# Kernel tuning notes

Hardware: AMD Instinct MI355X
Metric: run time of the kernel (lower is better)

Reference implementation:

```python
import jax, jax.numpy as jnp
import numpy as np


def setup_inputs() -> dict:
    key = jax.random.key(0)
    ks = jax.random.split(key, 16)
    N, F_in, C, E = 50000, 128, 64, 800000
    H = 2 * C      # hidden width of first GCN layer = 128
    P = 128        # num_proj_hidden
    K = 3          # cluster_num (hardcoded in GRACE)

    def lin(kw, fan_in, fan_out):
        # torch Linear default init: U(-1/sqrt(fan_in), 1/sqrt(fan_in))
        bound = 1.0 / np.sqrt(fan_in)
        return jax.random.uniform(kw, (fan_in, fan_out), jnp.float32, -bound, bound)

    inp = {
        "x1": jax.random.normal(ks[0], (N, F_in), jnp.float32),
        "edge_index1": jax.random.randint(ks[1], (2, E), 0, N, jnp.int64 if jax.config.jax_enable_x64 else jnp.int32),
        "x2": jax.random.normal(ks[2], (N, F_in), jnp.float32),
        "edge_index2": jax.random.randint(ks[3], (2, E), 0, N, jnp.int64 if jax.config.jax_enable_x64 else jnp.int32),
        # encoder GCN layers
        "W1": lin(ks[4], F_in, H), "b1": jnp.zeros((H,), jnp.float32),
        "W2": lin(ks[5], H, C),    "b2": jnp.zeros((C,), jnp.float32),
        # instance projector: Linear(C,C) -> ReLU -> Linear(C,P)
        "Wp1": lin(ks[6], C, C), "bp1": jnp.zeros((C,), jnp.float32),
        "Wp2": lin(ks[7], C, P), "bp2": jnp.zeros((P,), jnp.float32),
        # cluster projector: Linear(C,C) -> ReLU -> Linear(C,K) -> Softmax
        "Wc1": lin(ks[8], C, C), "bc1": jnp.zeros((C,), jnp.float32),
        "Wc2": lin(ks[9], C, K), "bc2": jnp.zeros((K,), jnp.float32),
    }
    return inp


def _gcn_encoder(x, edge_index, W1, b1, W2, b2):
    N = x.shape[0]
    loop = jnp.arange(N, dtype=edge_index.dtype)
    row = jnp.concatenate([edge_index[0], loop])  # message sources (x_j)
    col = jnp.concatenate([edge_index[1], loop])  # aggregation targets
    deg = jax.ops.segment_sum(jnp.ones_like(col, jnp.float32), col, num_segments=N)
    dinv = jax.lax.rsqrt(deg)  # deg >= 1 due to self loops
    norm = dinv[row] * dinv[col]  # [E+N]

    def layer(h, W, b):
        h = h @ W  # transform first (PyG GCNConv), [N, F_out]
        msg = h[row] * norm[:, None]  # gather + scale, [E+N, F_out]
        return jax.ops.segment_sum(msg, col, num_segments=N) + b

    h = jax.nn.relu(layer(x, W1, b1))
    h = jax.nn.relu(layer(h, W2, b2))
    return h


def _l2norm(z, eps=1e-12):
    # matches F.normalize(z, dim=1): x / max(||x||, eps)
    n = jnp.sqrt(jnp.sum(z * z, axis=1, keepdims=True))
    return z / jnp.maximum(n, eps)


def reference(x1, edge_index1, x2, edge_index2,
              W1, b1, W2, b2, Wp1, bp1, Wp2, bp2, Wc1, bc1, Wc2, bc2):
    z1 = _gcn_encoder(x1, edge_index1, W1, b1, W2, b2)
    z2 = _gcn_encoder(x2, edge_index2, W1, b1, W2, b2)

    inst = lambda z: _l2norm(jax.nn.relu(z @ Wp1 + bp1) @ Wp2 + bp2)
    clus = lambda z: jax.nn.softmax(jax.nn.relu(z @ Wc1 + bc1) @ Wc2 + bc2, axis=1)

    z_i = inst(z1)
    z_j = inst(z2)
    c_i = clus(z1)
    c_j = clus(z2)
    return (z_i, z_j, c_i, c_j)
```

## Files before the change

kernel.cpp:

```cpp
#include <hip/hip_runtime.h>
#include <cstdint>
#include <cstddef>

using u16 = unsigned short;
using u32 = unsigned int;

typedef __bf16 bf16x8 __attribute__((ext_vector_type(8)));
typedef float  f32x4  __attribute__((ext_vector_type(4)));

__device__ __forceinline__ float bf2f(u16 b) { union { u32 i; float f; } v; v.i = ((u32)b) << 16; return v.f; }
__device__ __forceinline__ u16 f2bf(float f) { __bf16 b = (__bf16)f; return __builtin_bit_cast(u16, b); }
__device__ __forceinline__ float bflo(u32 u) { union { u32 i; float f; } v; v.i = u << 16; return v.f; }
__device__ __forceinline__ float bfhi(u32 u) { union { u32 i; float f; } v; v.i = u & 0xffff0000u; return v.f; }
__device__ __forceinline__ u32 pack2(float a, float b) { return (u32)f2bf(a) | ((u32)f2bf(b) << 16); }

__device__ __forceinline__ void dot2acc(float& acc, u32 hv, u32 sel) {
    asm("v_dot2_f32_bf16 %0, %1, %2, %0" : "+v"(acc) : "v"(hv), "v"(sel));
}

__device__ __forceinline__ float loadx(const void* p, size_t i, int flag_bf16) {
    return flag_bf16 ? bf2f(((const u16*)p)[i]) : ((const float*)p)[i];
}
__device__ __forceinline__ void storex(void* p, size_t i, float v, int flag_bf16) {
    if (flag_bf16) ((u16*)p)[i] = f2bf(v);
    else           ((float*)p)[i] = v;
}

__device__ __forceinline__ bf16x8 load_afrag_ext(const void* A, size_t off, int flag) {
    if (flag) return *reinterpret_cast<const bf16x8*>((const u16*)A + off);
    const float* f = (const float*)A + off;
    float4 a = *reinterpret_cast<const float4*>(f);
    float4 b = *reinterpret_cast<const float4*>(f + 4);
    bf16x8 r;
    r[0] = (__bf16)a.x; r[1] = (__bf16)a.y; r[2] = (__bf16)a.z; r[3] = (__bf16)a.w;
    r[4] = (__bf16)b.x; r[5] = (__bf16)b.y; r[6] = (__bf16)b.z; r[7] = (__bf16)b.w;
    return r;
}

__global__ void k_detect(const u32* __restrict__ x, int* __restrict__ flag) {
    int lane = threadIdx.x;
    u32 u = x[lane];
    int e = (u >> 7) & 0xFF;
    int hit = (e >= 100 && e <= 145) ? 1 : 0;
    unsigned long long b = __ballot(hit);
    if (lane == 0) flag[0] = (__popcll(b) >= 32) ? 1 : 0;
}

struct ConvJob { const void* src; float* dst; int n; };
struct ConvJobs { ConvJob j[12]; };

__global__ void k_wconv(ConvJobs jobs, const int* __restrict__ flagp) {
    const int f = *flagp;
    const int stride = gridDim.x * blockDim.x;
    for (int s = 0; s < 12; ++s) {
        const ConvJob jb = jobs.j[s];
        for (int i = blockIdx.x * blockDim.x + threadIdx.x; i < jb.n; i += stride)
            jb.dst[i] = loadx(jb.src, i, f);
    }
}

struct TJob { const float* W; u16* WT; int K, NC; };
struct TJobs { TJob j[5]; };

__global__ void k_wtrans(TJobs jobs) {
    const int stride = gridDim.x * blockDim.x;
    for (int s = 0; s < 5; ++s) {
        const TJob jb = jobs.j[s];
        const int tot = jb.K * jb.NC;
        for (int i = blockIdx.x * blockDim.x + threadIdx.x; i < tot; i += stride) {
            int k = i / jb.NC, n = i - k * jb.NC;
            jb.WT[n * jb.K + k] = f2bf(jb.W[i]);
        }
    }
}

static const int CAPSH = 12;
static const int OVCAP = 65536;

__global__ __launch_bounds__(256) void k_bin(const int* __restrict__ ei0, const int* __restrict__ ei1,
                                             int* __restrict__ cur, u32* __restrict__ stage,
                                             int2* __restrict__ ov, int* __restrict__ ocnt,
                                             int E, int NB, int nblk) {
    const int g = blockIdx.y;
    const int* ei = g ? ei1 : ei0;
    const int chunk = (E + nblk - 1) / nblk;
    const int e0 = blockIdx.x * chunk;
    const int e1 = (e0 + chunk < E) ? e0 + chunk : E;
    const int tid = threadIdx.x;
    __shared__ int h[512];
    __shared__ int lb[512];
    for (int i = tid; i < NB; i += 256) h[i] = 0;
    __syncthreads();
    for (int e = e0 + tid; e < e1; e += 256) {
        int d = __builtin_nontemporal_load(ei + E + e);
        atomicAdd(&h[d >> 7], 1);
    }
    __syncthreads();
    for (int b = tid; b < NB; b += 256) {
        int c = h[b];
        lb[b] = c ? atomicAdd(&cur[g * NB + b], c) : 0;
    }
    __syncthreads();
    for (int i = tid; i < NB; i += 256) h[i] = 0;
    __syncthreads();
    for (int e = e0 + tid; e < e1; e += 256) {
        int s = __builtin_nontemporal_load(ei + e);
        int d = ei[E + e];
        int b = d >> 7;
        int p = lb[b] + atomicAdd(&h[b], 1);
        if (p < (1 << CAPSH)) {
            stage[((size_t)(g * NB + b) << CAPSH) + p] = (u32)s | ((u32)(d & 127) << 16);
        } else {
            int oi = atomicAdd(ocnt, 1);
            if (oi < OVCAP) ov[oi] = make_int2(s, d | (g << 24));
        }
    }
}

__global__ __launch_bounds__(256) void k_bscan(const int* __restrict__ cur, const int2* __restrict__ ov,
                                               const int* __restrict__ ocnt, int* __restrict__ bbase,
                                               int* __restrict__ rowptr, int N, int E, int NB) {
    __shared__ int tot[2][512];
    const int tid = threadIdx.x;
    for (int g = 0; g < 2; ++g)
        for (int i = tid; i < 512; i += 256) {
            int s = 0;
            if (i < NB) {
                int cv = cur[g * NB + i];
                s = (cv < (1 << CAPSH)) ? cv : (1 << CAPSH);
            }
            tot[g][i] = s;
        }
    __syncthreads();
    int no = *ocnt; if (no > OVCAP) no = OVCAP;
    for (int i = tid; i < no; i += 256) {
        int y = ov[i].y;
        atomicAdd(&tot[y >> 24][(y & 0xFFFFFF) >> 7], 1);
    }
    __syncthreads();
    int o00 = tot[0][tid], o01 = tot[0][tid + 256];
    int o10 = tot[1][tid], o11 = tot[1][tid + 256];
    for (int off = 1; off < 512; off <<= 1) {
        int a0 = tot[0][tid]       + ((tid >= off)       ? tot[0][tid - off]       : 0);
        int a1 = tot[0][tid + 256] + ((tid + 256 >= off) ? tot[0][tid + 256 - off] : 0);
        int b0 = tot[1][tid]       + ((tid >= off)       ? tot[1][tid - off]       : 0);
        int b1 = tot[1][tid + 256] + ((tid + 256 >= off) ? tot[1][tid + 256 - off] : 0);
        __syncthreads();
        tot[0][tid] = a0; tot[0][tid + 256] = a1;
        tot[1][tid] = b0; tot[1][tid + 256] = b1;
        __syncthreads();
    }
    if (tid < NB)       { bbase[tid]            = tot[0][tid] - o00;       bbase[NB + tid]       = tot[1][tid] - o10; }
    if (tid + 256 < NB) { bbase[tid + 256]      = tot[0][tid + 256] - o01; bbase[NB + tid + 256] = tot[1][tid + 256] - o11; }
    if (tid == 0) {
        rowptr[N] = E;
        rowptr[(size_t)(N + 1) + N] = E;
    }
}

__global__ __launch_bounds__(256) void k_scatter(const int* __restrict__ cur, const u32* __restrict__ stage,
                                                 const int2* __restrict__ ov, const int* __restrict__ ocnt,
                                                 const int* __restrict__ bbase, int* __restrict__ rowptr,
                                                 float* __restrict__ dinv, int* __restrict__ csr,
                                                 int N, int E, int NB) {
    const int g = blockIdx.y, b = blockIdx.x, tid = threadIdx.x;
    const int lo = b << 7;
    int R = N - lo; if (R > 128) R = 128;
    __shared__ int hist[128], scn[128], curs[128];
    if (tid < 128) hist[tid] = 0;
    __syncthreads();
    int cv = cur[g * NB + b];
    const int n = (cv < (1 << CAPSH)) ? cv : (1 << CAPSH);
    const u32* sp = stage + ((size_t)(g * NB + b) << CAPSH);
    for (int i = tid; i < n; i += 256) atomicAdd(&hist[sp[i] >> 16], 1);
    int no = *ocnt; if (no > OVCAP) no = OVCAP;
    for (int i = tid; i < no; i += 256) {
        int y = ov[i].y;
        if ((y >> 24) != g) continue;
        int d = y & 0xFFFFFF;
        if (d >= lo && d < lo + 128) atomicAdd(&hist[d - lo], 1);
    }
    __syncthreads();
    int orig = (tid < 128) ? hist[tid] : 0;
    if (tid < 128) scn[tid] = orig;
    __syncthreads();
    for (int off = 1; off < 128; off <<= 1) {
        int v = 0;
        if (tid < 128) v = scn[tid] + ((tid >= off) ? scn[tid - off] : 0);
        __syncthreads();
        if (tid < 128) scn[tid] = v;
        __syncthreads();
    }
    const int base = bbase[g * NB + b];
    if (tid < R) {
        int ex = base + scn[tid] - orig;
        rowptr[(size_t)g * (N + 1) + lo + tid] = ex;
        curs[tid] = ex;
        dinv[(size_t)g * N + lo + tid] = rsqrtf((float)(orig + 1));
    }
    __syncthreads();
    int* out = csr + (size_t)g * E;
    for (int i = tid; i < n; i += 256) {
        u32 v = sp[i];
        int pos = atomicAdd(&curs[v >> 16], 1);
        out[pos] = (int)(v & 0xFFFFu);
    }
    for (int i = tid; i < no; i += 256) {
        int y = ov[i].y;
        if ((y >> 24) != g) continue;
        int d = y & 0xFFFFFF;
        if (d >= lo && d < lo + 128) {
            int pos = atomicAdd(&curs[d - lo], 1);
            out[pos] = ov[i].x;
        }
    }
}

template <int K, int NC, bool AEXT, bool BIAS, bool RELU, bool NORM, bool OEXT, bool SCALE, int ARS>
__global__ __launch_bounds__(256) void k_mgemm(const void* __restrict__ A0, const void* __restrict__ A1,
                                               size_t astride, const u16* __restrict__ WT,
                                               const float* __restrict__ bias, void* __restrict__ outv,
                                               size_t out_off, size_t ostride, int M,
                                               const int* __restrict__ flagp,
                                               const float* __restrict__ dvp) {
    constexpr int NT = NC / 16;
    constexpr int KI = K / 32;
    constexpr int RS = (ARS == 0) ? K : ARS;
    const int flag = *flagp;
    const int g = blockIdx.y;
    const void* Av = g ? A1 : A0;
    const int lane = threadIdx.x & 63;
    const int wave = threadIdx.x >> 6;
    const int q = lane >> 4;
    const int c = lane & 15;
    const int m0 = blockIdx.x * 64 + wave * 16;
    int arow = m0 + c;
    if (arow > M - 1) arow = M - 1;
    const size_t abase = (size_t)g * astride + (size_t)arow * RS;

    bf16x8 afr[KI];
#pragma unroll
    for (int ki = 0; ki < KI; ++ki) {
        size_t off = abase + (size_t)ki * 32 + q * 8;
        if (AEXT) afr[ki] = load_afrag_ext(Av, off, flag);
        else      afr[ki] = *reinterpret_cast<const bf16x8*>((const u16*)Av + off);
    }

    f32x4 acc[NT];
#pragma unroll
    for (int t = 0; t < NT; ++t) acc[t] = (f32x4){0.f, 0.f, 0.f, 0.f};

#pragma unroll
    for (int ki = 0; ki < KI; ++ki) {
#pragma unroll
        for (int t = 0; t < NT; ++t) {
            const u16* bptr = WT + (size_t)(t * 16 + c) * K + ki * 32 + q * 8;
            bf16x8 bfr = *reinterpret_cast<const bf16x8*>(bptr);
            acc[t] = __builtin_amdgcn_mfma_f32_16x16x32_bf16(afr[ki], bfr, acc[t], 0, 0, 0);
        }
    }

#pragma unroll
    for (int t = 0; t < NT; ++t) {
        float bv = BIAS ? bias[t * 16 + c] : 0.f;
#pragma unroll
        for (int r = 0; r < 4; ++r) {
            float v = acc[t][r] + bv;
            if (RELU) v = fmaxf(v, 0.f);
            acc[t][r] = v;
        }
    }

    if constexpr (NORM) {
        float ss[4] = {0.f, 0.f, 0.f, 0.f};
#pragma unroll
        for (int t = 0; t < NT; ++t)
#pragma unroll
            for (int r = 0; r < 4; ++r) ss[r] += acc[t][r] * acc[t][r];
#pragma unroll
        for (int r = 0; r < 4; ++r) {
#pragma unroll
            for (int m = 1; m < 16; m <<= 1) ss[r] += __shfl_xor(ss[r], m, 64);
            float s = 1.f / fmaxf(sqrtf(ss[r]), 1e-12f);
#pragma unroll
            for (int t = 0; t < NT; ++t) acc[t][r] *= s;
        }
    }

    const size_t obase = out_off + (size_t)g * ostride;
#pragma unroll
    for (int r = 0; r < 4; ++r) {
        const int grow = m0 + q * 4 + r;
        if (grow < M) {
            float sc = 1.f;
            if constexpr (SCALE) sc = dvp[(size_t)g * M + grow];
#pragma unroll
            for (int t = 0; t < NT; ++t) {
                float v = SCALE ? acc[t][r] * sc : acc[t][r];
                size_t oi = obase + (size_t)grow * NC + t * 16 + c;
                if (OEXT) storex(outv, oi, v, flag);
                else      ((u16*)outv)[oi] = f2bf(v);
            }
        }
    }
}

__global__ __launch_bounds__(256) void k_agg128(const u32* __restrict__ H, const int* __restrict__ rowptr,
                                                const int* __restrict__ csr, const float* __restrict__ dinv,
                                                const float* __restrict__ bias, u32* __restrict__ out,
                                                int N, int E, int Q) {
    const u32 SL = 0x00003f80u, SH = 0x3f800000u;
    const int bid = blockIdx.x;
    const int role = bid & 7;
    const int g = role >> 2;
    const int sub = role & 3;
    const int nl = (bid >> 3) * 4 + (threadIdx.x >> 6);
    if (nl >= Q) return;
    const int node = sub * Q + nl;
    if (node >= N) return;
    const int lane = threadIdx.x & 63;
    const int half = lane >> 5;
    const int w = lane & 31;
    const u32* h2 = H + (size_t)g * N * 64 + 2 * w;
    const int* rp = rowptr + (size_t)g * (N + 1);
    const int* cs = csr + (size_t)g * E;
    const float dn = dinv[(size_t)g * N + node];
    int e = rp[node];
    const int end = rp[node + 1];
    float a0 = 0.f, a1 = 0.f, a2 = 0.f, a3 = 0.f;
    if (half == 0) {
        uint2 sv = *reinterpret_cast<const uint2*>(h2 + (size_t)node * 64);
        dot2acc(a0, sv.x, SL); dot2acc(a1, sv.x, SH);
        dot2acc(a2, sv.y, SL); dot2acc(a3, sv.y, SH);
    }
    while (e < end) {
        int cnt = end - e; if (cnt > 64) cnt = 64;
        int my = (lane < cnt) ? cs[e + lane] : 0;
        int j = 0;
        for (; j + 8 <= cnt; j += 8) {
            int s0 = __shfl(my, j + half, 64);
            int s1 = __shfl(my, j + 2 + half, 64);
            int s2 = __shfl(my, j + 4 + half, 64);
            int s3 = __shfl(my, j + 6 + half, 64);
            uint2 h0 = *reinterpret_cast<const uint2*>(h2 + (size_t)s0 * 64);
            uint2 h1 = *reinterpret_cast<const uint2*>(h2 + (size_t)s1 * 64);
            uint2 hh2 = *reinterpret_cast<const uint2*>(h2 + (size_t)s2 * 64);
            uint2 h3 = *reinterpret_cast<const uint2*>(h2 + (size_t)s3 * 64);
            dot2acc(a0, h0.x, SL); dot2acc(a1, h0.x, SH); dot2acc(a2, h0.y, SL); dot2acc(a3, h0.y, SH);
            dot2acc(a0, h1.x, SL); dot2acc(a1, h1.x, SH); dot2acc(a2, h1.y, SL); dot2acc(a3, h1.y, SH);
            dot2acc(a0, hh2.x, SL); dot2acc(a1, hh2.x, SH); dot2acc(a2, hh2.y, SL); dot2acc(a3, hh2.y, SH);
            dot2acc(a0, h3.x, SL); dot2acc(a1, h3.x, SH); dot2acc(a2, h3.y, SL); dot2acc(a3, h3.y, SH);
        }
        for (; j < cnt; j += 2) {
            int idx = j + half;
            int src = __shfl(my, idx < cnt ? idx : 0, 64);
            if (idx < cnt) {
                uint2 hv = *reinterpret_cast<const uint2*>(h2 + (size_t)src * 64);
                dot2acc(a0, hv.x, SL); dot2acc(a1, hv.x, SH);
                dot2acc(a2, hv.y, SL); dot2acc(a3, hv.y, SH);
            }
        }
        e += cnt;
    }
    a0 += __shfl_xor(a0, 32, 64);
    a1 += __shfl_xor(a1, 32, 64);
    a2 += __shfl_xor(a2, 32, 64);
    a3 += __shfl_xor(a3, 32, 64);
    float x = half ? a2 : a0;
    float y = half ? a3 : a1;
    const int c0 = 4 * w + 2 * half;
    float r0 = fmaxf(x * dn + bias[c0], 0.f);
    float r1 = fmaxf(y * dn + bias[c0 + 1], 0.f);
    out[((size_t)g * N + node) * 64 + 2 * w + half] = pack2(r0, r1);
}

__global__ __launch_bounds__(256) void k_agg64(const u32* __restrict__ H, const int* __restrict__ rowptr,
                                               const int* __restrict__ csr, const float* __restrict__ dinv,
                                               const float* __restrict__ bias, u32* __restrict__ out,
                                               int N, int E, int Q) {
    const u32 SL = 0x00003f80u, SH = 0x3f800000u;
    const int bid = blockIdx.x;
    const int role = bid & 7;
    const int g = role >> 2;
    const int sub = role & 3;
    const int nl = (bid >> 3) * 4 + (threadIdx.x >> 6);
    if (nl >= Q) return;
    const int node = sub * Q + nl;
    if (node >= N) return;
    const int lane = threadIdx.x & 63;
    const int quad = lane >> 4;
    const int w = lane & 15;
    const u32* h2 = H + (size_t)g * N * 32 + 2 * w;
    const int* rp = rowptr + (size_t)g * (N + 1);
    const int* cs = csr + (size_t)g * E;
    const float dn = dinv[(size_t)g * N + node];
    int e = rp[node];
    const int end = rp[node + 1];
    float a0 = 0.f, a1 = 0.f, a2 = 0.f, a3 = 0.f;
    if (quad == 0) {
        uint2 sv = *reinterpret_cast<const uint2*>(h2 + (size_t)node * 32);
        dot2acc(a0, sv.x, SL); dot2acc(a1, sv.x, SH);
        dot2acc(a2, sv.y, SL); dot2acc(a3, sv.y, SH);
    }
    while (e < end) {
        int cnt = end - e; if (cnt > 64) cnt = 64;
        int my = (lane < cnt) ? cs[e + lane] : 0;
        int j = 0;
        for (; j + 16 <= cnt; j += 16) {
            int s0 = __shfl(my, j + quad, 64);
            int s1 = __shfl(my, j + 4 + quad, 64);
            int s2 = __shfl(my, j + 8 + quad, 64);
            int s3 = __shfl(my, j + 12 + quad, 64);
            uint2 h0 = *reinterpret_cast<const uint2*>(h2 + (size_t)s0 * 32);
            uint2 h1 = *reinterpret_cast<const uint2*>(h2 + (size_t)s1 * 32);
            uint2 hh2 = *reinterpret_cast<const uint2*>(h2 + (size_t)s2 * 32);
            uint2 h3 = *reinterpret_cast<const uint2*>(h2 + (size_t)s3 * 32);
            dot2acc(a0, h0.x, SL); dot2acc(a1, h0.x, SH); dot2acc(a2, h0.y, SL); dot2acc(a3, h0.y, SH);
            dot2acc(a0, h1.x, SL); dot2acc(a1, h1.x, SH); dot2acc(a2, h1.y, SL); dot2acc(a3, h1.y, SH);
            dot2acc(a0, hh2.x, SL); dot2acc(a1, hh2.x, SH); dot2acc(a2, hh2.y, SL); dot2acc(a3, hh2.y, SH);
            dot2acc(a0, h3.x, SL); dot2acc(a1, h3.x, SH); dot2acc(a2, h3.y, SL); dot2acc(a3, h3.y, SH);
        }
        for (; j < cnt; j += 4) {
            int idx = j + quad;
            int src = __shfl(my, idx < cnt ? idx : 0, 64);
            if (idx < cnt) {
                uint2 hv = *reinterpret_cast<const uint2*>(h2 + (size_t)src * 32);
                dot2acc(a0, hv.x, SL); dot2acc(a1, hv.x, SH);
                dot2acc(a2, hv.y, SL); dot2acc(a3, hv.y, SH);
            }
        }
        e += cnt;
    }
    a0 += __shfl_xor(a0, 16, 64); a0 += __shfl_xor(a0, 32, 64);
    a1 += __shfl_xor(a1, 16, 64); a1 += __shfl_xor(a1, 32, 64);
    a2 += __shfl_xor(a2, 16, 64); a2 += __shfl_xor(a2, 32, 64);
    a3 += __shfl_xor(a3, 16, 64); a3 += __shfl_xor(a3, 32, 64);
    if (quad < 2) {
        float x = quad ? a2 : a0;
        float y = quad ? a3 : a1;
        const int c0 = 4 * w + 2 * quad;
        float r0 = fmaxf(x * dn + bias[c0], 0.f);
        float r1 = fmaxf(y * dn + bias[c0 + 1], 0.f);
        out[((size_t)g * N + node) * 32 + 2 * w + quad] = pack2(r0, r1);
    }
}

__global__ __launch_bounds__(256) void k_clus(const u16* __restrict__ v, const float* __restrict__ Wc2,
                                              const float* __restrict__ bc2, void* __restrict__ outv,
                                              size_t out_off, size_t ostride, int N,
                                              const int* __restrict__ flagp) {
    const int g = blockIdx.y;
    const int node = blockIdx.x * 4 + (threadIdx.x >> 6);
    if (node >= N) return;
    const int flag = *flagp;
    const int lane = threadIdx.x & 63;
    float ul = bf2f(v[((size_t)g * N + node) * 128 + 64 + lane]);
    float a0 = ul * Wc2[lane * 3 + 0];
    float a1 = ul * Wc2[lane * 3 + 1];
    float a2 = ul * Wc2[lane * 3 + 2];
#pragma unroll
    for (int m = 1; m < 64; m <<= 1) {
        a0 += __shfl_xor(a0, m, 64);
        a1 += __shfl_xor(a1, m, 64);
        a2 += __shfl_xor(a2, m, 64);
    }
    a0 += bc2[0]; a1 += bc2[1]; a2 += bc2[2];
    float mx = fmaxf(a0, fmaxf(a1, a2));
    float e0 = expf(a0 - mx), e1 = expf(a1 - mx), e2 = expf(a2 - mx);
    float inv = 1.f / (e0 + e1 + e2);
    if (lane < 3) {
        float r = (lane == 0) ? e0 : ((lane == 1) ? e1 : e2);
        storex(outv, out_off + (size_t)g * ostride + (size_t)node * 3 + lane, r * inv, flag);
    }
}

extern "C" void kernel_launch(void* const* d_in, const int* in_sizes, int n_in,
                              void* d_out, int out_size, void* d_ws, size_t ws_size,
                              hipStream_t stream) {
    const int N = in_sizes[0] / 128;
    const int E = in_sizes[1] / 2;
    const int* ei0 = (const int*)d_in[1];
    const int* ei1 = (const int*)d_in[3];
    const int NB = (N + 127) >> 7;

    size_t off = 0;
    auto alloc = [&](size_t bytes) -> void* {
        void* p = (char*)d_ws + off;
        off += (bytes + 255) & ~(size_t)255;
        return p;
    };
    int* flag = (int*)alloc(256);
    const int wcnt[12] = {128 * 128, 128, 128 * 64, 64, 64 * 64, 64, 64 * 128, 128, 64 * 64, 64, 64 * 3, 3};
    float* wf[12];
    for (int i = 0; i < 12; ++i) {
        if (i == 5) { wf[5] = (float*)alloc(128 * 4); continue; }
        if (i == 9) { wf[9] = wf[5] + 64; continue; }
        wf[i] = (float*)alloc((size_t)wcnt[i] * 4);
    }
    float* b1f = wf[1]; float* b2f = wf[3]; float* bpcf = wf[5]; float* bp2f = wf[7];
    float* Wc2f = wf[10]; float* bc2f = wf[11];
    u16* W1T  = (u16*)alloc(128 * 128 * 2);
    u16* W2T  = (u16*)alloc(64 * 128 * 2);
    u16* Wp1T = (u16*)alloc(64 * 64 * 2);
    u16* Wc1T = (u16*)alloc(64 * 64 * 2);
    u16* Wp2T = (u16*)alloc(128 * 64 * 2);
    u16* WpcT = Wp1T;

    const int ncell = 2 * NB;
    int* cur    = (int*)alloc((size_t)(ncell + 1) * 4);
    int* ocnt   = cur + ncell;
    int2* ov    = (int2*)alloc((size_t)OVCAP * 8);
    u32* stage  = (u32*)alloc(((size_t)ncell << CAPSH) * 4);
    int* bbase  = (int*)alloc((size_t)2 * NB * 4);
    int* rowptr = (int*)alloc((size_t)2 * (N + 1) * 4);
    float* dinv = (float*)alloc((size_t)2 * N * 4);
    int* csr    = (int*)alloc((size_t)2 * E * 4);
    u16* A1 = (u16*)alloc((size_t)2 * N * 128 * 2);
    u16* H2 = A1;
    u16* Qb = (u16*)alloc((size_t)2 * N * 128 * 2);
    u16* U2 = Qb;
    u16* Z  = (u16*)alloc((size_t)2 * N * 64 * 2);
    (void)ws_size; (void)n_in; (void)out_size;

    k_detect<<<1, 64, 0, stream>>>((const u32*)d_in[0], flag);
    ConvJobs jobs;
    for (int i = 0; i < 12; ++i) jobs.j[i] = ConvJob{d_in[4 + i], wf[i], wcnt[i]};
    k_wconv<<<64, 256, 0, stream>>>(jobs, flag);
    TJobs tj;
    tj.j[0] = TJob{wf[0], W1T, 128, 128};
    tj.j[1] = TJob{wf[2], W2T, 128, 64};
    tj.j[2] = TJob{wf[4], Wp1T, 64, 64};
    tj.j[3] = TJob{wf[8], Wc1T, 64, 64};
    tj.j[4] = TJob{wf[6], Wp2T, 64, 128};
    k_wtrans<<<40, 256, 0, stream>>>(tj);

    hipMemsetAsync(cur, 0, (size_t)(ncell + 1) * 4, stream);
    const int NBLK = 128;
    k_bin<<<dim3(NBLK, 2), 256, 0, stream>>>(ei0, ei1, cur, stage, ov, ocnt, E, NB, NBLK);
    k_bscan<<<1, 256, 0, stream>>>(cur, ov, ocnt, bbase, rowptr, N, E, NB);
    k_scatter<<<dim3(NB, 2), 256, 0, stream>>>(cur, stage, ov, ocnt, bbase, rowptr, dinv, csr, N, E, NB);

    const dim3 gM((N + 63) / 64, 2);
    const dim3 gA((N + 3) / 4, 2);
    const int Q = (N + 3) / 4;
    const dim3 gAgg(8 * ((Q + 3) / 4));

    k_mgemm<128, 128, true, false, false, false, false, true, 0><<<gM, 256, 0, stream>>>(
        d_in[0], d_in[2], 0, W1T, nullptr, A1, 0, (size_t)N * 128, N, flag, dinv);
    k_agg128<<<gAgg, 256, 0, stream>>>((const u32*)A1, rowptr, csr, dinv, b1f, (u32*)Qb, N, E, Q);
    k_mgemm<128, 64, false, false, false, false, false, true, 0><<<gM, 256, 0, stream>>>(
        Qb, Qb, (size_t)N * 128, W2T, nullptr, H2, 0, (size_t)N * 64, N, flag, dinv);
    k_agg64<<<gAgg, 256, 0, stream>>>((const u32*)H2, rowptr, csr, dinv, b2f, (u32*)Z, N, E, Q);

    k_mgemm<64, 128, false, true, true, false, false, false, 0><<<gM, 256, 0, stream>>>(
        Z, Z, (size_t)N * 64, WpcT, bpcf, U2, 0, (size_t)N * 128, N, flag, nullptr);
    k_mgemm<64, 128, false, true, false, true, true, false, 128><<<gM, 256, 0, stream>>>(
        U2, U2, (size_t)N * 128, Wp2T, bp2f, d_out, 0, (size_t)N * 128, N, flag, nullptr);
    k_clus<<<gA, 256, 0, stream>>>(U2, Wc2f, bc2f, d_out,
                                   (size_t)2 * N * 128, (size_t)N * 3, N, flag);
}
```

Baseline: 404.8 us.

## Fuse first-layer aggregation with second-layer GEMM via LDS tile and MFMA

The layer-1 aggregation kernel now handles 16 nodes per block (4 per wave). It writes the ReLU'd bf16 rows into a swizzled LDS tile, then multiplies that tile by W2T with MFMA 16x16x32 and scales by dinv to produce H2 directly. This removes a separate GEMM launch and the write and re-read of the 128-wide intermediate, and H2 moves to the Qb buffer. In exchange each wave processes four nodes sequentially, which may lower parallelism and latency hiding in the gather, and a block barrier is added.

```diff
diff --git a/kernel.cpp b/kernel.cpp
--- a/kernel.cpp
+++ b/kernel.cpp
@@ -305,73 +305,107 @@
     }
 }
 
-__global__ __launch_bounds__(256) void k_agg128(const u32* __restrict__ H, const int* __restrict__ rowptr,
-                                                const int* __restrict__ csr, const float* __restrict__ dinv,
-                                                const float* __restrict__ bias, u32* __restrict__ out,
-                                                int N, int E, int Q) {
+__global__ __launch_bounds__(256) void k_agg128f(const u32* __restrict__ H, const int* __restrict__ rowptr,
+                                                 const int* __restrict__ csr, const float* __restrict__ dinv,
+                                                 const float* __restrict__ bias, const u16* __restrict__ W2T,
+                                                 u16* __restrict__ H2, int N, int E, int Q) {
     const u32 SL = 0x00003f80u, SH = 0x3f800000u;
     const int bid = blockIdx.x;
     const int role = bid & 7;
     const int g = role >> 2;
     const int sub = role & 3;
-    const int nl = (bid >> 3) * 4 + (threadIdx.x >> 6);
-    if (nl >= Q) return;
-    const int node = sub * Q + nl;
-    if (node >= N) return;
+    const int blk16 = bid >> 3;
     const int lane = threadIdx.x & 63;
+    const int wv = threadIdx.x >> 6;
     const int half = lane >> 5;
     const int w = lane & 31;
     const u32* h2 = H + (size_t)g * N * 64 + 2 * w;
     const int* rp = rowptr + (size_t)g * (N + 1);
     const int* cs = csr + (size_t)g * E;
-    const float dn = dinv[(size_t)g * N + node];
-    int e = rp[node];
-    const int end = rp[node + 1];
-    float a0 = 0.f, a1 = 0.f, a2 = 0.f, a3 = 0.f;
-    if (half == 0) {
-        uint2 sv = *reinterpret_cast<const uint2*>(h2 + (size_t)node * 64);
-        dot2acc(a0, sv.x, SL); dot2acc(a1, sv.x, SH);
-        dot2acc(a2, sv.y, SL); dot2acc(a3, sv.y, SH);
-    }
-    while (e < end) {
-        int cnt = end - e; if (cnt > 64) cnt = 64;
-        int my = (lane < cnt) ? cs[e + lane] : 0;
-        int j = 0;
-        for (; j + 8 <= cnt; j += 8) {
-            int s0 = __shfl(my, j + half, 64);
-            int s1 = __shfl(my, j + 2 + half, 64);
-            int s2 = __shfl(my, j + 4 + half, 64);
-            int s3 = __shfl(my, j + 6 + half, 64);
-            uint2 h0 = *reinterpret_cast<const uint2*>(h2 + (size_t)s0 * 64);
-            uint2 h1 = *reinterpret_cast<const uint2*>(h2 + (size_t)s1 * 64);
-            uint2 hh2 = *reinterpret_cast<const uint2*>(h2 + (size_t)s2 * 64);
-            uint2 h3 = *reinterpret_cast<const uint2*>(h2 + (size_t)s3 * 64);
-            dot2acc(a0, h0.x, SL); dot2acc(a1, h0.x, SH); dot2acc(a2, h0.y, SL); dot2acc(a3, h0.y, SH);
-            dot2acc(a0, h1.x, SL); dot2acc(a1, h1.x, SH); dot2acc(a2, h1.y, SL); dot2acc(a3, h1.y, SH);
-            dot2acc(a0, hh2.x, SL); dot2acc(a1, hh2.x, SH); dot2acc(a2, hh2.y, SL); dot2acc(a3, hh2.y, SH);
-            dot2acc(a0, h3.x, SL); dot2acc(a1, h3.x, SH); dot2acc(a2, h3.y, SL); dot2acc(a3, h3.y, SH);
-        }
-        for (; j < cnt; j += 2) {
-            int idx = j + half;
-            int src = __shfl(my, idx < cnt ? idx : 0, 64);
-            if (idx < cnt) {
-                uint2 hv = *reinterpret_cast<const uint2*>(h2 + (size_t)src * 64);
-                dot2acc(a0, hv.x, SL); dot2acc(a1, hv.x, SH);
-                dot2acc(a2, hv.y, SL); dot2acc(a3, hv.y, SH);
+
+    __shared__ __align__(16) u32 qlds[16][64];
+
+#pragma unroll
+    for (int i = 0; i < 4; ++i) {
+        const int tr = wv * 4 + i;
+        const int nl = blk16 * 16 + tr;
+        const bool valid = (nl < Q) && (sub * Q + nl < N);
+        const int node = valid ? sub * Q + nl : 0;
+        const float dn = dinv[(size_t)g * N + node];
+        int e = rp[node];
+        const int end = rp[node + 1];
+        float a0 = 0.f, a1 = 0.f, a2 = 0.f, a3 = 0.f;
+        if (half == 0) {
+            uint2 sv = *reinterpret_cast<const uint2*>(h2 + (size_t)node * 64);
+            dot2acc(a0, sv.x, SL); dot2acc(a1, sv.x, SH);
+            dot2acc(a2, sv.y, SL); dot2acc(a3, sv.y, SH);
+        }
+        while (e < end) {
+            int cnt = end - e; if (cnt > 64) cnt = 64;
+            int my = (lane < cnt) ? cs[e + lane] : 0;
+            int j = 0;
+            for (; j + 8 <= cnt; j += 8) {
+                int s0 = __shfl(my, j + half, 64);
+                int s1 = __shfl(my, j + 2 + half, 64);
+                int s2 = __shfl(my, j + 4 + half, 64);
+                int s3 = __shfl(my, j + 6 + half, 64);
+                uint2 h0 = *reinterpret_cast<const uint2*>(h2 + (size_t)s0 * 64);
+                uint2 h1 = *reinterpret_cast<const uint2*>(h2 + (size_t)s1 * 64);
+                uint2 hh2 = *reinterpret_cast<const uint2*>(h2 + (size_t)s2 * 64);
+                uint2 h3 = *reinterpret_cast<const uint2*>(h2 + (size_t)s3 * 64);
+                dot2acc(a0, h0.x, SL); dot2acc(a1, h0.x, SH); dot2acc(a2, h0.y, SL); dot2acc(a3, h0.y, SH);
+                dot2acc(a0, h1.x, SL); dot2acc(a1, h1.x, SH); dot2acc(a2, h1.y, SL); dot2acc(a3, h1.y, SH);
+                dot2acc(a0, hh2.x, SL); dot2acc(a1, hh2.x, SH); dot2acc(a2, hh2.y, SL); dot2acc(a3, hh2.y, SH);
+                dot2acc(a0, h3.x, SL); dot2acc(a1, h3.x, SH); dot2acc(a2, h3.y, SL); dot2acc(a3, h3.y, SH);
             }
-        }
-        e += cnt;
-    }
-    a0 += __shfl_xor(a0, 32, 64);
-    a1 += __shfl_xor(a1, 32, 64);
-    a2 += __shfl_xor(a2, 32, 64);
-    a3 += __shfl_xor(a3, 32, 64);
-    float x = half ? a2 : a0;
-    float y = half ? a3 : a1;
-    const int c0 = 4 * w + 2 * half;
-    float r0 = fmaxf(x * dn + bias[c0], 0.f);
-    float r1 = fmaxf(y * dn + bias[c0 + 1], 0.f);
-    out[((size_t)g * N + node) * 64 + 2 * w + half] = pack2(r0, r1);
+            for (; j < cnt; j += 2) {
+                int idx = j + half;
+                int src = __shfl(my, idx < cnt ? idx : 0, 64);
+                if (idx < cnt) {
+                    uint2 hv = *reinterpret_cast<const uint2*>(h2 + (size_t)src * 64);
+                    dot2acc(a0, hv.x, SL); dot2acc(a1, hv.x, SH);
+                    dot2acc(a2, hv.y, SL); dot2acc(a3, hv.y, SH);
+                }
+            }
+            e += cnt;
+        }
+        a0 += __shfl_xor(a0, 32, 64);
+        a1 += __shfl_xor(a1, 32, 64);
+        a2 += __shfl_xor(a2, 32, 64);
+        a3 += __shfl_xor(a3, 32, 64);
+        float x = half ? a2 : a0;
+        float y = half ? a3 : a1;
+        const int c0 = 4 * w + 2 * half;
+        float r0 = fmaxf(x * dn + bias[c0], 0.f);
+        float r1 = fmaxf(y * dn + bias[c0 + 1], 0.f);
+        const int jc = 2 * w + half;
+        qlds[tr][jc ^ ((tr & 7) << 2)] = pack2(r0, r1);
+    }
+    __syncthreads();
+
+    const int q = lane >> 4;
+    const int c = lane & 15;
+    f32x4 acc = (f32x4){0.f, 0.f, 0.f, 0.f};
+#pragma unroll
+    for (int ki = 0; ki < 4; ++ki) {
+        const int base = (ki * 16 + q * 4) ^ ((c & 7) << 2);
+        bf16x8 afr = *reinterpret_cast<const bf16x8*>(&qlds[c][base]);
+        const u16* bptr = W2T + (size_t)(wv * 16 + c) * 128 + ki * 32 + q * 8;
+        bf16x8 bfr = *reinterpret_cast<const bf16x8*>(bptr);
+        acc = __builtin_amdgcn_mfma_f32_16x16x32_bf16(afr, bfr, acc, 0, 0, 0);
+    }
+#pragma unroll
+    for (int r = 0; r < 4; ++r) {
+        const int tr = q * 4 + r;
+        const int nl = blk16 * 16 + tr;
+        if (nl < Q) {
+            const int node = sub * Q + nl;
+            if (node < N) {
+                float sc = dinv[(size_t)g * N + node];
+                H2[(size_t)(g * N + node) * 64 + wv * 16 + c] = f2bf(acc[r] * sc);
+            }
+        }
+    }
 }
 
 __global__ __launch_bounds__(256) void k_agg64(const u32* __restrict__ H, const int* __restrict__ rowptr,
@@ -516,8 +550,8 @@
     float* dinv = (float*)alloc((size_t)2 * N * 4);
     int* csr    = (int*)alloc((size_t)2 * E * 4);
     u16* A1 = (u16*)alloc((size_t)2 * N * 128 * 2);
-    u16* H2 = A1;
     u16* Qb = (u16*)alloc((size_t)2 * N * 128 * 2);
+    u16* H2 = Qb;
     u16* U2 = Qb;
     u16* Z  = (u16*)alloc((size_t)2 * N * 64 * 2);
     (void)ws_size; (void)n_in; (void)out_size;
@@ -544,12 +578,11 @@
     const dim3 gA((N + 3) / 4, 2);
     const int Q = (N + 3) / 4;
     const dim3 gAgg(8 * ((Q + 3) / 4));
+    const dim3 gAgg16(8 * ((Q + 15) / 16));
 
     k_mgemm<128, 128, true, false, false, false, false, true, 0><<<gM, 256, 0, stream>>>(
         d_in[0], d_in[2], 0, W1T, nullptr, A1, 0, (size_t)N * 128, N, flag, dinv);
-    k_agg128<<<gAgg, 256, 0, stream>>>((const u32*)A1, rowptr, csr, dinv, b1f, (u32*)Qb, N, E, Q);
-    k_mgemm<128, 64, false, false, false, false, false, true, 0><<<gM, 256, 0, stream>>>(
-        Qb, Qb, (size_t)N * 128, W2T, nullptr, H2, 0, (size_t)N * 64, N, flag, dinv);
+    k_agg128f<<<gAgg16, 256, 0, stream>>>((const u32*)A1, rowptr, csr, dinv, b1f, W2T, H2, N, E, Q);
     k_agg64<<<gAgg, 256, 0, stream>>>((const u32*)H2, rowptr, csr, dinv, b2f, (u32*)Z, N, E, Q);
 
     k_mgemm<64, 128, false, true, true, false, false, false, 0><<<gM, 256, 0, stream>>>(
```

New measurement: 396.0 us. 1.02x faster.
